# Performance work log

Measured on AMD Instinct MI355X. Metric: run time of the kernel, lower is better.

Reference implementation:

```python
import jax, jax.numpy as jnp
import numpy as np

N = 50000      # nodes
E = 800000     # edges (avg degree 16)
F0 = 3         # node feature dim
EF = 3         # edge feature dim
C = 4          # num classes


def _lin_params(k, din, dout):
    k1, k2 = jax.random.split(k)
    s = 1.0 / np.sqrt(din)
    W = jax.random.uniform(k1, (dout, din), jnp.float32, -s, s)
    b = jax.random.uniform(k2, (dout,), jnp.float32, -s, s)
    return W, b


def setup_inputs() -> dict:
    key = jax.random.key(0)
    ks = jax.random.split(key, 8)
    x = jax.random.normal(ks[0], (N, F0), jnp.float32)
    edge_index = jax.random.randint(ks[1], (2, E), 0, N, jnp.int32)
    edge_attr = jax.random.uniform(ks[2], (E, EF), dtype=jnp.float32)
    W1, b1 = _lin_params(ks[3], 2 * F0 + EF, 128)
    W2, b2 = _lin_params(ks[4], 2 * 128 + EF, 64)
    W3, b3 = _lin_params(ks[5], 2 * 64 + EF, 32)
    Wc, bc = _lin_params(ks[6], 32, C)
    return dict(x=x, edge_index=edge_index, edge_attr=edge_attr,
                W1=W1, b1=b1, W2=W2, b2=b2, W3=W3, b3=b3, Wc=Wc, bc=bc)


def _edgeconv(x, src, dst, ea, W, b, n):
    # message = Linear(cat([x_i, x_j, edge_attr])); aggregated by scatter-add to dst (x_i side).
    # Split W so the node-side matmuls happen once per node instead of per edge.
    f = x.shape[1]
    Wi, Wj, We = W[:, :f], W[:, f:2 * f], W[:, 2 * f:]
    ai = x @ Wi.T   # [N, out]
    aj = x @ Wj.T   # [N, out]
    msg = ai[dst] + aj[src] + ea @ We.T + b  # [E_aug, out]
    return jax.ops.segment_sum(msg, dst, num_segments=n)


def reference(x, edge_index, edge_attr, W1, b1, W2, b2, W3, b3, Wc, bc):
    n = x.shape[0]
    loops = jnp.arange(n, dtype=edge_index.dtype)
    src = jnp.concatenate([edge_index[0], loops])  # x_j indices
    dst = jnp.concatenate([edge_index[1], loops])  # x_i indices (aggregation targets)
    ea = jnp.concatenate([edge_attr, jnp.zeros((n, edge_attr.shape[1]), edge_attr.dtype)])
    h = jax.nn.relu(_edgeconv(x, src, dst, ea, W1, b1, n))
    h = jax.nn.relu(_edgeconv(h, src, dst, ea, W2, b2, n))
    h = _edgeconv(h, src, dst, ea, W3, b3, n)  # no relu after conv3 in the original
    logits = h @ Wc.T + bc
    return jax.nn.log_softmax(logits, axis=1)
```

## Files before the change

kernel.cpp:

```cpp
#include <hip/hip_runtime.h>
#include <math.h>


static inline size_t align256(size_t x) { return (x + 255) & ~size_t(255); }

typedef unsigned short ushort_t;
using frag8  = __attribute__((ext_vector_type(8))) short;
using f32x4v = __attribute__((ext_vector_type(4))) float;

__device__ inline unsigned short f2bf(float f) {
    unsigned u = __float_as_uint(f);
    unsigned r = (u + 0x7fffu + ((u >> 16) & 1u)) >> 16;
    return (unsigned short)r;
}
__device__ inline float bflo(unsigned u) { return __uint_as_float(u << 16); }
__device__ inline float bfhi(unsigned u) { return __uint_as_float(u & 0xffff0000u); }


__global__ __launch_bounds__(256) void build_count(
    const int* __restrict__ ei, int* __restrict__ count,
    int* __restrict__ pos, int E)
{
    int e4 = (blockIdx.x * 256 + threadIdx.x) * 4;
    if (e4 >= E) return;
    if (e4 + 3 < E) {
        int4 d = *(const int4*)(ei + E + e4);
        int4 po;
        po.x = atomicAdd(&count[d.x], 1);
        po.y = atomicAdd(&count[d.y], 1);
        po.z = atomicAdd(&count[d.z], 1);
        po.w = atomicAdd(&count[d.w], 1);
        *(int4*)(pos + e4) = po;
    } else {
        for (int e = e4; e < E; ++e)
            pos[e] = atomicAdd(&count[ei[E + e]], 1);
    }
}

__global__ __launch_bounds__(256) void scan_pass1(
    const int* __restrict__ count, int* __restrict__ rowstart,
    int* __restrict__ bsum, int n)
{
    __shared__ int sh[256];
    const int tid = threadIdx.x;
    const int base = blockIdx.x * 1024 + tid * 4;
    int v0 = 0, v1 = 0, v2 = 0, v3 = 0;
    if (base + 3 < n) {
        int4 c = *(const int4*)(count + base);
        v0 = c.x; v1 = c.y; v2 = c.z; v3 = c.w;
    } else {
        if (base + 0 < n) v0 = count[base + 0];
        if (base + 1 < n) v1 = count[base + 1];
        if (base + 2 < n) v2 = count[base + 2];
        if (base + 3 < n) v3 = count[base + 3];
    }
    int tsum = v0 + v1 + v2 + v3;
    sh[tid] = tsum;
    __syncthreads();
    for (int off = 1; off < 256; off <<= 1) {
        int t = (tid >= off) ? sh[tid - off] : 0;
        __syncthreads();
        sh[tid] += t;
        __syncthreads();
    }
    int excl = sh[tid] - tsum;
    int p0 = excl + v0, p1 = p0 + v1, p2 = p1 + v2, p3 = p2 + v3;
    if (base + 0 < n) rowstart[base + 1] = p0;
    if (base + 1 < n) rowstart[base + 2] = p1;
    if (base + 2 < n) rowstart[base + 3] = p2;
    if (base + 3 < n) rowstart[base + 4] = p3;
    if (tid == 255) bsum[blockIdx.x] = sh[255];
}

__global__ __launch_bounds__(64) void scan_pass2(
    const int* __restrict__ bsum, int* __restrict__ bexcl, int nb)
{
    int lane = threadIdx.x;
    int own = (lane < nb) ? bsum[lane] : 0;
    int x = own;
    for (int off = 1; off < 64; off <<= 1) {
        int t = __shfl_up(x, off);
        if (lane >= off) x += t;
    }
    bexcl[lane] = x - own;
}

__global__ __launch_bounds__(256) void scan_pass3(
    int* __restrict__ rowstart, const int* __restrict__ bexcl, int n)
{
    int j = blockIdx.x * 256 + threadIdx.x;
    if (j > n) return;
    if (j == 0) { rowstart[0] = 0; return; }
    int b = (j - 1) >> 10;
    if (b > 0) rowstart[j] += bexcl[b];
}

__global__ __launch_bounds__(256) void csr_scatter(
    const int* __restrict__ ei, const float* __restrict__ ea,
    const int* __restrict__ pos, const int* __restrict__ rowstart,
    uint2* __restrict__ csrp, int E)
{
    int e4 = (blockIdx.x * 256 + threadIdx.x) * 4;
    if (e4 >= E) return;
    if (e4 + 3 < E) {
        int4 s = *(const int4*)(ei + e4);
        int4 d = *(const int4*)(ei + E + e4);
        int4 po = *(const int4*)(pos + e4);
        float4 a = *(const float4*)(ea + (size_t)e4 * 3);
        float4 b = *(const float4*)(ea + (size_t)e4 * 3 + 4);
        float4 c = *(const float4*)(ea + (size_t)e4 * 3 + 8);
        float ev[12] = { a.x, a.y, a.z, a.w, b.x, b.y, b.z, b.w, c.x, c.y, c.z, c.w };
        int sv[4] = { s.x, s.y, s.z, s.w };
        int dv[4] = { d.x, d.y, d.z, d.w };
        int pv[4] = { po.x, po.y, po.z, po.w };
        #pragma unroll
        for (int r = 0; r < 4; ++r) {
            uint2 p;
            p.x = (unsigned)f2bf(ev[r * 3 + 0]) | ((unsigned)f2bf(ev[r * 3 + 1]) << 16);
            p.y = (unsigned)f2bf(ev[r * 3 + 2]) | ((unsigned)sv[r] << 16);
            csrp[rowstart[dv[r]] + pv[r]] = p;
        }
    } else {
        for (int e = e4; e < E; ++e) {
            uint2 p;
            p.x = (unsigned)f2bf(ea[e * 3 + 0]) | ((unsigned)f2bf(ea[e * 3 + 1]) << 16);
            p.y = (unsigned)f2bf(ea[e * 3 + 2]) | ((unsigned)ei[e] << 16);
            csrp[rowstart[ei[E + e]] + pos[e]] = p;
        }
    }
}


__global__ __launch_bounds__(256) void prep_collapse(
    const float* __restrict__ W3, const float* __restrict__ b3,
    const float* __restrict__ Wc, const float* __restrict__ bc,
    float* __restrict__ AB, float* __restrict__ consts)
{
    int t = threadIdx.x;
    for (int idx = t; idx < 512; idx += 256) {
        int j = idx >> 6, k = idx & 63;
        int jj = j & 3;
        int base = (j >= 4) ? 64 : 0;
        float s = 0.f;
        #pragma unroll
        for (int c = 0; c < 32; ++c)
            s += Wc[jj * 32 + c] * W3[c * 131 + base + k];
        AB[idx] = s;
    }
    if (t < 4) {
        float db = 0.f;
        for (int c = 0; c < 32; ++c) db += Wc[t * 32 + c] * b3[c];
        consts[t] = db;
        consts[4 + t] = bc[t];
        for (int q = 0; q < 3; ++q) {
            float s = 0.f;
            for (int c = 0; c < 32; ++c) s += Wc[t * 32 + c] * W3[c * 131 + 128 + q];
            consts[8 + t * 3 + q] = s;
        }
    }
}


__global__ __launch_bounds__(256) void h1_fused(
    const float* __restrict__ x, const float* __restrict__ W1,
    const float* __restrict__ b1, const int* __restrict__ rowstart,
    const uint2* __restrict__ csrp, float4* __restrict__ eagg4,
    ushort_t* __restrict__ h1, int n_nodes)
{
    __shared__ float sM[10 * 128];
    const int tid = threadIdx.x;
    for (int t = tid; t < 1280; t += 256) {
        int k = t >> 7, c = t & 127;
        sM[t] = (k < 9) ? W1[c * 9 + k] : b1[c];
    }
    __syncthreads();

    int wl = tid & 63;
    int grp = wl >> 3, ch8 = wl & 7;
    int n = blockIdx.x * 32 + (tid >> 6) * 8 + grp;
    if (n >= n_nodes) return;

    int s0 = rowstart[n], s1 = rowstart[n + 1];
    float xx = 0.f, xy = 0.f, xz = 0.f, ex = 0.f, ey = 0.f, ez = 0.f;
    for (int i = s0 + ch8; i < s1; i += 8) {
        uint2 p = csrp[i];
        int s = (int)(p.y >> 16);
        ex += bflo(p.x); ey += bfhi(p.x); ez += bflo(p.y);
        const float* xp = x + (size_t)s * 3;
        xx += xp[0]; xy += xp[1]; xz += xp[2];
    }
    #pragma unroll
    for (int off = 1; off < 8; off <<= 1) {
        xx += __shfl_xor(xx, off); xy += __shfl_xor(xy, off); xz += __shfl_xor(xz, off);
        ex += __shfl_xor(ex, off); ey += __shfl_xor(ey, off); ez += __shfl_xor(ez, off);
    }

    float deg = (float)(s1 - s0 + 1);
    float x0 = x[n * 3], x1 = x[n * 3 + 1], x2 = x[n * 3 + 2];
    float v[10] = { deg * x0, deg * x1, deg * x2,
                    x0 + xx, x1 + xy, x2 + xz,
                    ex, ey, ez, deg };
    int cb = ch8 * 16;
    #pragma unroll
    for (int g = 0; g < 2; ++g) {
        float hv[8];
        #pragma unroll
        for (int q = 0; q < 8; ++q) {
            int c = cb + g * 8 + q;
            float h = 0.f;
            #pragma unroll
            for (int k = 0; k < 10; ++k) h += v[k] * sM[k * 128 + c];
            hv[q] = fmaxf(h, 0.f);
        }
        uint4 u;
        u.x = (unsigned)f2bf(hv[0]) | ((unsigned)f2bf(hv[1]) << 16);
        u.y = (unsigned)f2bf(hv[2]) | ((unsigned)f2bf(hv[3]) << 16);
        u.z = (unsigned)f2bf(hv[4]) | ((unsigned)f2bf(hv[5]) << 16);
        u.w = (unsigned)f2bf(hv[6]) | ((unsigned)f2bf(hv[7]) << 16);
        *(uint4*)(h1 + (size_t)n * 128 + cb + g * 8) = u;
    }
    if (ch8 == 0) eagg4[n] = make_float4(ex, ey, ez, 0.f);
}


__global__ __launch_bounds__(256) void gemm_mfma(
    const ushort_t* __restrict__ h1, const float* __restrict__ W2,
    float* __restrict__ AI2, ushort_t* __restrict__ AJ2, int n_nodes)
{
    constexpr int KP = 136;
    __shared__ ushort_t sB[128 * KP];

    const int tid = threadIdx.x;
    for (int t = tid; t < 128 * 128; t += 256) {
        int jg = t >> 7, k = t & 127;
        float w = (jg < 64) ? W2[jg * 259 + k] : W2[(jg - 64) * 259 + 128 + k];
        sB[jg * KP + k] = f2bf(w);
    }
    __syncthreads();

    const int wave = tid >> 6, lane = tid & 63;
    const int m = lane & 15, quad = lane >> 4;
    const int mwave = blockIdx.x * 64 + wave * 16;

    int arow = mwave + m;
    int arow_c = arow < n_nodes ? arow : (n_nodes - 1);

    frag8 a[4];
    #pragma unroll
    for (int ks = 0; ks < 4; ++ks)
        a[ks] = *(const frag8*)(h1 + (size_t)arow_c * 128 + ks * 32 + quad * 8);

    f32x4v acc[8];
    #pragma unroll
    for (int t = 0; t < 8; ++t) acc[t] = (f32x4v)(0.f);

    #pragma unroll
    for (int t = 0; t < 8; ++t) {
        #pragma unroll
        for (int ks = 0; ks < 4; ++ks) {
            frag8 b = *(const frag8*)(sB + (t * 16 + m) * KP + ks * 32 + quad * 8);
            acc[t] = __builtin_amdgcn_mfma_f32_16x16x32_bf16(a[ks], b, acc[t], 0, 0, 0);
        }
    }

    #pragma unroll
    for (int reg = 0; reg < 4; ++reg) {
        int grow = mwave + quad * 4 + reg;
        if (grow >= n_nodes) continue;
        #pragma unroll
        for (int t = 0; t < 4; ++t)
            AI2[(size_t)grow * 64 + t * 16 + m] = acc[t][reg];
        #pragma unroll
        for (int t = 4; t < 8; ++t)
            AJ2[(size_t)grow * 64 + (t - 4) * 16 + m] = f2bf(acc[t][reg]);
    }
}


__global__ __launch_bounds__(256) void gather2(
    const float* __restrict__ AI2, const ushort_t* __restrict__ AJ2,
    const float* __restrict__ W2, const float* __restrict__ b2,
    const float4* __restrict__ eagg4, const int* __restrict__ rowstart,
    const uint2* __restrict__ csrp, const float* __restrict__ AB,
    float* __restrict__ U, float* __restrict__ Z, int n_nodes)
{
    __shared__ float sAB[512];
    __shared__ float sWe[192];
    const int tid = threadIdx.x;
    for (int t = tid; t < 512; t += 256) sAB[t] = AB[t];
    for (int t = tid; t < 192; t += 256) {
        int c = t / 3, q = t % 3;
        sWe[t] = W2[c * 259 + 256 + q];
    }
    __syncthreads();

    int wl = tid & 63;
    int grp = wl >> 3, ch8 = wl & 7;
    int n = blockIdx.x * 32 + (tid >> 6) * 8 + grp;
    if (n >= n_nodes) return;

    int s0 = rowstart[n], s1 = rowstart[n + 1];
    int trip = s1 - s0;

    float acc[8];
    #pragma unroll
    for (int q = 0; q < 8; ++q) acc[q] = 0.f;

    int myidx = 0;
    for (int it = 0; it < trip; ++it) {
        if ((it & 7) == 0) {
            int j = s0 + it + ch8;
            if (j >= s1) j = s1 - 1;
            myidx = (int)(csrp[j].y >> 16);
        }
        int s = __shfl(myidx, grp * 8 + (it & 7));
        uint4 u = *(const uint4*)(AJ2 + (size_t)s * 64 + ch8 * 8);
        acc[0] += bflo(u.x); acc[1] += bfhi(u.x);
        acc[2] += bflo(u.y); acc[3] += bfhi(u.y);
        acc[4] += bflo(u.z); acc[5] += bfhi(u.z);
        acc[6] += bflo(u.w); acc[7] += bfhi(u.w);
    }

    float deg = (float)(trip + 1);
    float4 e4 = eagg4[n];
    const float* aip = AI2 + (size_t)n * 64 + ch8 * 8;
    float4 aiA = *(const float4*)(aip);
    float4 aiB = *(const float4*)(aip + 4);
    uint4 su = *(const uint4*)(AJ2 + (size_t)n * 64 + ch8 * 8);
    float ajs[8] = { bflo(su.x), bfhi(su.x), bflo(su.y), bfhi(su.y),
                     bflo(su.z), bfhi(su.z), bflo(su.w), bfhi(su.w) };
    float4 bA = *(const float4*)(b2 + ch8 * 8);
    float4 bB = *(const float4*)(b2 + ch8 * 8 + 4);
    float av[8] = { aiA.x, aiA.y, aiA.z, aiA.w, aiB.x, aiB.y, aiB.z, aiB.w };
    float bv[8] = { bA.x, bA.y, bA.z, bA.w, bB.x, bB.y, bB.z, bB.w };
    float r[8];
    #pragma unroll
    for (int q = 0; q < 8; ++q) {
        int c = ch8 * 8 + q;
        float we = sWe[c * 3] * e4.x + sWe[c * 3 + 1] * e4.y + sWe[c * 3 + 2] * e4.z;
        r[q] = fmaxf(deg * (av[q] + bv[q]) + ajs[q] + we + acc[q], 0.f);
    }
    float pj[8];
    #pragma unroll
    for (int j = 0; j < 8; ++j) {
        float4 wA = *(const float4*)(sAB + j * 64 + ch8 * 8);
        float4 wB = *(const float4*)(sAB + j * 64 + ch8 * 8 + 4);
        pj[j] = r[0] * wA.x + r[1] * wA.y + r[2] * wA.z + r[3] * wA.w
              + r[4] * wB.x + r[5] * wB.y + r[6] * wB.z + r[7] * wB.w;
    }
    #pragma unroll
    for (int off = 1; off < 8; off <<= 1)
        #pragma unroll
        for (int j = 0; j < 8; ++j) pj[j] += __shfl_xor(pj[j], off);

    if (ch8 == 0) {
        *(float4*)(U + (size_t)n * 4) = make_float4(pj[0], pj[1], pj[2], pj[3]);
        *(float4*)(Z + (size_t)n * 4) = make_float4(pj[4], pj[5], pj[6], pj[7]);
    }
}


__global__ __launch_bounds__(256) void final_softmax(
    const float* __restrict__ U, const float* __restrict__ Z,
    const float4* __restrict__ eagg4, const int* __restrict__ rowstart,
    const uint2* __restrict__ csrp, const float* __restrict__ consts,
    float* __restrict__ out, int n_nodes)
{
    int wl = threadIdx.x & 63;
    int grp = wl >> 3, ch8 = wl & 7;
    int n = blockIdx.x * 32 + (threadIdx.x >> 6) * 8 + grp;
    if (n >= n_nodes) return;

    int s0 = rowstart[n], s1 = rowstart[n + 1];
    float ax = 0.f, ay = 0.f, az = 0.f, aw = 0.f;
    for (int i = s0 + ch8; i < s1; i += 8) {
        int s = (int)(csrp[i].y >> 16);
        float4 z = *(const float4*)(Z + (size_t)s * 4);
        ax += z.x; ay += z.y; az += z.z; aw += z.w;
    }
    #pragma unroll
    for (int off = 1; off < 8; off <<= 1) {
        ax += __shfl_xor(ax, off); ay += __shfl_xor(ay, off);
        az += __shfl_xor(az, off); aw += __shfl_xor(aw, off);
    }
    if (ch8 != 0) return;

    float deg = (float)(s1 - s0 + 1);
    float4 u = *(const float4*)(U + (size_t)n * 4);
    float4 zs = *(const float4*)(Z + (size_t)n * 4);
    float4 e4 = eagg4[n];
    float av[4] = { ax + zs.x, ay + zs.y, az + zs.z, aw + zs.w };
    float uv[4] = { u.x, u.y, u.z, u.w };
    float lg[4];
    #pragma unroll
    for (int j = 0; j < 4; ++j) {
        lg[j] = deg * (uv[j] + consts[j]) + av[j] + consts[4 + j]
              + consts[8 + j * 3] * e4.x + consts[9 + j * 3] * e4.y
              + consts[10 + j * 3] * e4.z;
    }
    float m = fmaxf(fmaxf(lg[0], lg[1]), fmaxf(lg[2], lg[3]));
    float lse = logf(expf(lg[0] - m) + expf(lg[1] - m) + expf(lg[2] - m) + expf(lg[3] - m));
    *(float4*)(out + (size_t)n * 4) =
        make_float4(lg[0] - m - lse, lg[1] - m - lse, lg[2] - m - lse, lg[3] - m - lse);
}


extern "C" void kernel_launch(void* const* d_in, const int* in_sizes, int n_in,
                              void* d_out, int out_size, void* d_ws, size_t ws_size,
                              hipStream_t stream)
{
    const float* x    = (const float*)d_in[0];
    const int*   ei   = (const int*)  d_in[1];
    const float* ea   = (const float*)d_in[2];
    const float* W1   = (const float*)d_in[3];
    const float* b1   = (const float*)d_in[4];
    const float* W2   = (const float*)d_in[5];
    const float* b2   = (const float*)d_in[6];
    const float* W3   = (const float*)d_in[7];
    const float* b3   = (const float*)d_in[8];
    const float* Wc   = (const float*)d_in[9];
    const float* bc   = (const float*)d_in[10];
    float* out = (float*)d_out;

    const int N = in_sizes[0] / 3;
    const int E = in_sizes[1] / 2;

    char* ws = (char*)d_ws;
    size_t off = 0;
    int*    count    = (int*)(ws + off);            off = align256(off + (size_t)N * 4);
    int*    pos      = (int*)(ws + off);            off = align256(off + (size_t)E * 4);
    int*    rowstart = (int*)(ws + off);            off = align256(off + (size_t)(N + 1) * 4);
    uint2*  csrp     = (uint2*)(ws + off);          off = align256(off + (size_t)E * 8);
    int*    bsum     = (int*)(ws + off);            off = align256(off + 256);
    int*    bexcl    = (int*)(ws + off);            off = align256(off + 256);
    float*  AB       = (float*)(ws + off);          off = align256(off + 512 * 4);
    float*  consts   = (float*)(ws + off);          off = align256(off + 32 * 4);
    float4* eagg4    = (float4*)(ws + off);         off = align256(off + (size_t)N * 16);
    ushort_t* h1buf  = (ushort_t*)(ws + off);       off = align256(off + (size_t)N * 128 * 2);
    float*  AI2      = (float*)(ws + off);          off = align256(off + (size_t)N * 64 * 4);
    ushort_t* AJ2    = (ushort_t*)(ws + off);       off = align256(off + (size_t)N * 64 * 2);
    float*  Ubuf     = (float*)(ws + off);          off = align256(off + (size_t)N * 16);
    float*  Zbuf     = (float*)(ws + off);          off = align256(off + (size_t)N * 16);
    (void)ws_size;

    hipMemsetAsync(count, 0, (size_t)N * 4, stream);

    const int eb4 = ((E + 3) / 4 + 255) / 256;
    build_count<<<eb4, 256, 0, stream>>>(ei, count, pos, E);

    const int nb1 = (N + 1023) / 1024;
    scan_pass1<<<nb1, 256, 0, stream>>>(count, rowstart, bsum, N);
    scan_pass2<<<1, 64, 0, stream>>>(bsum, bexcl, nb1);
    scan_pass3<<<(N + 1 + 255) / 256, 256, 0, stream>>>(rowstart, bexcl, N);
    csr_scatter<<<eb4, 256, 0, stream>>>(ei, ea, pos, rowstart, csrp, E);

    prep_collapse<<<1, 256, 0, stream>>>(W3, b3, Wc, bc, AB, consts);

    const int gb = (N + 31) / 32;

    h1_fused<<<gb, 256, 0, stream>>>(x, W1, b1, rowstart, csrp, eagg4, h1buf, N);

    gemm_mfma<<<(N + 63) / 64, 256, 0, stream>>>(h1buf, W2, AI2, AJ2, N);
    gather2<<<gb, 256, 0, stream>>>(AI2, AJ2, W2, b2, eagg4, rowstart, csrp, AB, Ubuf, Zbuf, N);

    final_softmax<<<gb, 256, 0, stream>>>(Ubuf, Zbuf, eagg4, rowstart, csrp, consts, out, N);
}
```

Baseline: 203.4 us.

## Use atomic cursor CSR fill, padded x, and fp16 gather accumulation

The per-edge pos array written by build_count is dropped. csr_scatter now takes slots through atomicAdd on a per-node cursor that scan_pass3 initialises, which removes a 4-byte-per-edge write and read. x is repacked into float4 so neighbour gathers in h1_fused are single vector loads. AJ2 is stored as fp16, and gather2 accumulates neighbour rows with packed half8 adds, loading eight neighbours per index fetch. This trades accumulation precision, since fp16 can overflow or lose accuracy on sums over high-degree nodes, and it makes the order of edges within a CSR row nondeterministic.

```diff
diff --git a/kernel.cpp b/kernel.cpp
--- a/kernel.cpp
+++ b/kernel.cpp
@@ -7,6 +7,7 @@
 typedef unsigned short ushort_t;
 using frag8  = __attribute__((ext_vector_type(8))) short;
 using f32x4v = __attribute__((ext_vector_type(4))) float;
+using half8  = __attribute__((ext_vector_type(8))) _Float16;
 
 __device__ inline unsigned short f2bf(float f) {
     unsigned u = __float_as_uint(f);
@@ -18,22 +19,19 @@
 
 
 __global__ __launch_bounds__(256) void build_count(
-    const int* __restrict__ ei, int* __restrict__ count,
-    int* __restrict__ pos, int E)
+    const int* __restrict__ ei, int* __restrict__ count, int E)
 {
     int e4 = (blockIdx.x * 256 + threadIdx.x) * 4;
     if (e4 >= E) return;
     if (e4 + 3 < E) {
         int4 d = *(const int4*)(ei + E + e4);
-        int4 po;
-        po.x = atomicAdd(&count[d.x], 1);
-        po.y = atomicAdd(&count[d.y], 1);
-        po.z = atomicAdd(&count[d.z], 1);
-        po.w = atomicAdd(&count[d.w], 1);
-        *(int4*)(pos + e4) = po;
+        atomicAdd(&count[d.x], 1);
+        atomicAdd(&count[d.y], 1);
+        atomicAdd(&count[d.z], 1);
+        atomicAdd(&count[d.w], 1);
     } else {
         for (int e = e4; e < E; ++e)
-            pos[e] = atomicAdd(&count[ei[E + e]], 1);
+            atomicAdd(&count[ei[E + e]], 1);
     }
 }
 
@@ -86,46 +84,57 @@
 }
 
 __global__ __launch_bounds__(256) void scan_pass3(
-    int* __restrict__ rowstart, const int* __restrict__ bexcl, int n)
+    int* __restrict__ rowstart, const int* __restrict__ bexcl,
+    int* __restrict__ cursor, const float* __restrict__ x,
+    float4* __restrict__ xpad, int n)
 {
     int j = blockIdx.x * 256 + threadIdx.x;
     if (j > n) return;
-    if (j == 0) { rowstart[0] = 0; return; }
-    int b = (j - 1) >> 10;
-    if (b > 0) rowstart[j] += bexcl[b];
+    int rs;
+    if (j == 0) {
+        rs = 0;
+        rowstart[0] = 0;
+    } else {
+        int b = (j - 1) >> 10;
+        rs = rowstart[j];
+        if (b > 0) { rs += bexcl[b]; rowstart[j] = rs; }
+    }
+    if (j < n) {
+        cursor[j] = rs;
+        xpad[j] = make_float4(x[j * 3], x[j * 3 + 1], x[j * 3 + 2], 0.f);
+    }
 }
 
 __global__ __launch_bounds__(256) void csr_scatter(
     const int* __restrict__ ei, const float* __restrict__ ea,
-    const int* __restrict__ pos, const int* __restrict__ rowstart,
-    uint2* __restrict__ csrp, int E)
+    int* __restrict__ cursor, uint2* __restrict__ csrp, int E)
 {
     int e4 = (blockIdx.x * 256 + threadIdx.x) * 4;
     if (e4 >= E) return;
     if (e4 + 3 < E) {
         int4 s = *(const int4*)(ei + e4);
         int4 d = *(const int4*)(ei + E + e4);
-        int4 po = *(const int4*)(pos + e4);
         float4 a = *(const float4*)(ea + (size_t)e4 * 3);
         float4 b = *(const float4*)(ea + (size_t)e4 * 3 + 4);
         float4 c = *(const float4*)(ea + (size_t)e4 * 3 + 8);
         float ev[12] = { a.x, a.y, a.z, a.w, b.x, b.y, b.z, b.w, c.x, c.y, c.z, c.w };
         int sv[4] = { s.x, s.y, s.z, s.w };
         int dv[4] = { d.x, d.y, d.z, d.w };
-        int pv[4] = { po.x, po.y, po.z, po.w };
         #pragma unroll
         for (int r = 0; r < 4; ++r) {
             uint2 p;
             p.x = (unsigned)f2bf(ev[r * 3 + 0]) | ((unsigned)f2bf(ev[r * 3 + 1]) << 16);
             p.y = (unsigned)f2bf(ev[r * 3 + 2]) | ((unsigned)sv[r] << 16);
-            csrp[rowstart[dv[r]] + pv[r]] = p;
+            int slot = atomicAdd(&cursor[dv[r]], 1);
+            csrp[slot] = p;
         }
     } else {
         for (int e = e4; e < E; ++e) {
             uint2 p;
             p.x = (unsigned)f2bf(ea[e * 3 + 0]) | ((unsigned)f2bf(ea[e * 3 + 1]) << 16);
             p.y = (unsigned)f2bf(ea[e * 3 + 2]) | ((unsigned)ei[e] << 16);
-            csrp[rowstart[ei[E + e]] + pos[e]] = p;
+            int slot = atomicAdd(&cursor[ei[E + e]], 1);
+            csrp[slot] = p;
         }
     }
 }
@@ -162,7 +171,7 @@
 
 
 __global__ __launch_bounds__(256) void h1_fused(
-    const float* __restrict__ x, const float* __restrict__ W1,
+    const float4* __restrict__ xpad, const float* __restrict__ W1,
     const float* __restrict__ b1, const int* __restrict__ rowstart,
     const uint2* __restrict__ csrp, float4* __restrict__ eagg4,
     ushort_t* __restrict__ h1, int n_nodes)
@@ -186,8 +195,8 @@
         uint2 p = csrp[i];
         int s = (int)(p.y >> 16);
         ex += bflo(p.x); ey += bfhi(p.x); ez += bflo(p.y);
-        const float* xp = x + (size_t)s * 3;
-        xx += xp[0]; xy += xp[1]; xz += xp[2];
+        float4 xv = xpad[s];
+        xx += xv.x; xy += xv.y; xz += xv.z;
     }
     #pragma unroll
     for (int off = 1; off < 8; off <<= 1) {
@@ -196,9 +205,9 @@
     }
 
     float deg = (float)(s1 - s0 + 1);
-    float x0 = x[n * 3], x1 = x[n * 3 + 1], x2 = x[n * 3 + 2];
-    float v[10] = { deg * x0, deg * x1, deg * x2,
-                    x0 + xx, x1 + xy, x2 + xz,
+    float4 xs = xpad[n];
+    float v[10] = { deg * xs.x, deg * xs.y, deg * xs.z,
+                    xs.x + xx, xs.y + xy, xs.z + xz,
                     ex, ey, ez, deg };
     int cb = ch8 * 16;
     #pragma unroll
@@ -225,7 +234,7 @@
 
 __global__ __launch_bounds__(256) void gemm_mfma(
     const ushort_t* __restrict__ h1, const float* __restrict__ W2,
-    float* __restrict__ AI2, ushort_t* __restrict__ AJ2, int n_nodes)
+    float* __restrict__ AI2, _Float16* __restrict__ AJ2, int n_nodes)
 {
     constexpr int KP = 136;
     __shared__ ushort_t sB[128 * KP];
@@ -272,13 +281,13 @@
             AI2[(size_t)grow * 64 + t * 16 + m] = acc[t][reg];
         #pragma unroll
         for (int t = 4; t < 8; ++t)
-            AJ2[(size_t)grow * 64 + (t - 4) * 16 + m] = f2bf(acc[t][reg]);
+            AJ2[(size_t)grow * 64 + (t - 4) * 16 + m] = (_Float16)acc[t][reg];
     }
 }
 
 
 __global__ __launch_bounds__(256) void gather2(
-    const float* __restrict__ AI2, const ushort_t* __restrict__ AJ2,
+    const float* __restrict__ AI2, const _Float16* __restrict__ AJ2,
     const float* __restrict__ W2, const float* __restrict__ b2,
     const float4* __restrict__ eagg4, const int* __restrict__ rowstart,
     const uint2* __restrict__ csrp, const float* __restrict__ AB,
@@ -300,35 +309,32 @@
     if (n >= n_nodes) return;
 
     int s0 = rowstart[n], s1 = rowstart[n + 1];
-    int trip = s1 - s0;
-
+
+    half8 hacc = (half8)(_Float16)0.f;
+    for (int base = s0; base < s1; base += 8) {
+        int j = base + ch8;
+        if (j >= s1) j = s1 - 1;
+        int myidx = (int)(csrp[j].y >> 16);
+        int cnt = s1 - base; if (cnt > 8) cnt = 8;
+        #pragma unroll
+        for (int k = 0; k < 8; ++k) {
+            int s = __shfl(myidx, grp * 8 + k);
+            if (k < cnt) {
+                half8 v = *(const half8*)(AJ2 + (size_t)s * 64 + ch8 * 8);
+                hacc += v;
+            }
+        }
+    }
     float acc[8];
     #pragma unroll
-    for (int q = 0; q < 8; ++q) acc[q] = 0.f;
-
-    int myidx = 0;
-    for (int it = 0; it < trip; ++it) {
-        if ((it & 7) == 0) {
-            int j = s0 + it + ch8;
-            if (j >= s1) j = s1 - 1;
-            myidx = (int)(csrp[j].y >> 16);
-        }
-        int s = __shfl(myidx, grp * 8 + (it & 7));
-        uint4 u = *(const uint4*)(AJ2 + (size_t)s * 64 + ch8 * 8);
-        acc[0] += bflo(u.x); acc[1] += bfhi(u.x);
-        acc[2] += bflo(u.y); acc[3] += bfhi(u.y);
-        acc[4] += bflo(u.z); acc[5] += bfhi(u.z);
-        acc[6] += bflo(u.w); acc[7] += bfhi(u.w);
-    }
-
-    float deg = (float)(trip + 1);
+    for (int q = 0; q < 8; ++q) acc[q] = (float)hacc[q];
+
+    float deg = (float)(s1 - s0 + 1);
     float4 e4 = eagg4[n];
     const float* aip = AI2 + (size_t)n * 64 + ch8 * 8;
     float4 aiA = *(const float4*)(aip);
     float4 aiB = *(const float4*)(aip + 4);
-    uint4 su = *(const uint4*)(AJ2 + (size_t)n * 64 + ch8 * 8);
-    float ajs[8] = { bflo(su.x), bfhi(su.x), bflo(su.y), bfhi(su.y),
-                     bflo(su.z), bfhi(su.z), bflo(su.w), bfhi(su.w) };
+    half8 su = *(const half8*)(AJ2 + (size_t)n * 64 + ch8 * 8);
     float4 bA = *(const float4*)(b2 + ch8 * 8);
     float4 bB = *(const float4*)(b2 + ch8 * 8 + 4);
     float av[8] = { aiA.x, aiA.y, aiA.z, aiA.w, aiB.x, aiB.y, aiB.z, aiB.w };
@@ -338,7 +344,7 @@
     for (int q = 0; q < 8; ++q) {
         int c = ch8 * 8 + q;
         float we = sWe[c * 3] * e4.x + sWe[c * 3 + 1] * e4.y + sWe[c * 3 + 2] * e4.z;
-        r[q] = fmaxf(deg * (av[q] + bv[q]) + ajs[q] + we + acc[q], 0.f);
+        r[q] = fmaxf(deg * (av[q] + bv[q]) + (float)su[q] + we + acc[q], 0.f);
     }
     float pj[8];
     #pragma unroll
@@ -428,17 +434,18 @@
     char* ws = (char*)d_ws;
     size_t off = 0;
     int*    count    = (int*)(ws + off);            off = align256(off + (size_t)N * 4);
-    int*    pos      = (int*)(ws + off);            off = align256(off + (size_t)E * 4);
+    int*    cursor   = (int*)(ws + off);            off = align256(off + (size_t)N * 4);
     int*    rowstart = (int*)(ws + off);            off = align256(off + (size_t)(N + 1) * 4);
     uint2*  csrp     = (uint2*)(ws + off);          off = align256(off + (size_t)E * 8);
     int*    bsum     = (int*)(ws + off);            off = align256(off + 256);
     int*    bexcl    = (int*)(ws + off);            off = align256(off + 256);
     float*  AB       = (float*)(ws + off);          off = align256(off + 512 * 4);
     float*  consts   = (float*)(ws + off);          off = align256(off + 32 * 4);
+    float4* xpad     = (float4*)(ws + off);         off = align256(off + (size_t)N * 16);
     float4* eagg4    = (float4*)(ws + off);         off = align256(off + (size_t)N * 16);
     ushort_t* h1buf  = (ushort_t*)(ws + off);       off = align256(off + (size_t)N * 128 * 2);
     float*  AI2      = (float*)(ws + off);          off = align256(off + (size_t)N * 64 * 4);
-    ushort_t* AJ2    = (ushort_t*)(ws + off);       off = align256(off + (size_t)N * 64 * 2);
+    _Float16* AJ2    = (_Float16*)(ws + off);       off = align256(off + (size_t)N * 64 * 2);
     float*  Ubuf     = (float*)(ws + off);          off = align256(off + (size_t)N * 16);
     float*  Zbuf     = (float*)(ws + off);          off = align256(off + (size_t)N * 16);
     (void)ws_size;
@@ -446,19 +453,19 @@
     hipMemsetAsync(count, 0, (size_t)N * 4, stream);
 
     const int eb4 = ((E + 3) / 4 + 255) / 256;
-    build_count<<<eb4, 256, 0, stream>>>(ei, count, pos, E);
+    build_count<<<eb4, 256, 0, stream>>>(ei, count, E);
 
     const int nb1 = (N + 1023) / 1024;
     scan_pass1<<<nb1, 256, 0, stream>>>(count, rowstart, bsum, N);
     scan_pass2<<<1, 64, 0, stream>>>(bsum, bexcl, nb1);
-    scan_pass3<<<(N + 1 + 255) / 256, 256, 0, stream>>>(rowstart, bexcl, N);
-    csr_scatter<<<eb4, 256, 0, stream>>>(ei, ea, pos, rowstart, csrp, E);
+    scan_pass3<<<(N + 1 + 255) / 256, 256, 0, stream>>>(rowstart, bexcl, cursor, x, xpad, N);
+    csr_scatter<<<eb4, 256, 0, stream>>>(ei, ea, cursor, csrp, E);
 
     prep_collapse<<<1, 256, 0, stream>>>(W3, b3, Wc, bc, AB, consts);
 
     const int gb = (N + 31) / 32;
 
-    h1_fused<<<gb, 256, 0, stream>>>(x, W1, b1, rowstart, csrp, eagg4, h1buf, N);
+    h1_fused<<<gb, 256, 0, stream>>>(xpad, W1, b1, rowstart, csrp, eagg4, h1buf, N);
 
     gemm_mfma<<<(N + 63) / 64, 256, 0, stream>>>(h1buf, W2, AI2, AJ2, N);
     gather2<<<gb, 256, 0, stream>>>(AI2, AJ2, W2, b2, eagg4, rowstart, csrp, AB, Ubuf, Zbuf, N);
```

Result: slower. 252.5 us (+24.1%).
